# Kernel tuning notes

Hardware: AMD Instinct MI355X
Metric: run time of the kernel (lower is better)

## Reference

```python
import jax, jax.numpy as jnp
import numpy as np

H = 256  # hidden_size
B, LQ, LK = 4, 4096, 4096


def setup_inputs() -> dict:
    key = jax.random.key(0)
    ks = jax.random.split(key, 9)
    s = 1.0 / np.sqrt(H)
    return {
        "q": jax.random.normal(ks[0], (B, LQ, H), jnp.float32),
        "k": jax.random.normal(ks[1], (B, LK, H), jnp.float32),
        "v": jax.random.normal(ks[2], (B, LK, H), jnp.float32),
        "Wq": jax.random.uniform(ks[3], (H, H), jnp.float32, -s, s),
        "bq": jax.random.uniform(ks[4], (H,), jnp.float32, -s, s),
        "Wk": jax.random.uniform(ks[5], (H, H), jnp.float32, -s, s),
        "bk": jax.random.uniform(ks[6], (H,), jnp.float32, -s, s),
        "Wv": jax.random.uniform(ks[7], (H, H), jnp.float32, -s, s),
        "bv": jax.random.uniform(ks[8], (H,), jnp.float32, -s, s),
    }


def reference(q, k, v, Wq, bq, Wk, bk, Wv, bv):
    # Linear projections (torch Linear: x @ W.T + b)
    query = jnp.einsum('bsh,oh->bso', q, Wq) + bq
    keys = jnp.einsum('bsh,oh->bso', k, Wk) + bk
    values = jnp.einsum('bsh,oh->bso', v, Wv) + bv
    scores = jnp.einsum('bqh,bkh->bqk', query, keys) / jnp.sqrt(jnp.float32(H))
    weights = jax.nn.softmax(scores, axis=-1)
    context = jnp.einsum('bqk,bkh->bqh', weights, values)
    return context
```

## Files before the change

### kernel.cpp

```cpp
#include <hip/hip_runtime.h>
#include <hip/hip_bf16.h>
#include <stdint.h>

#define HD   256
#define SEQ  4096
#define NB   4
#define NTOK (NB * SEQ)
#define NEL  ((size_t)NTOK * HD)

typedef __hip_bfloat16 bf16;
typedef short    bf16x8  __attribute__((ext_vector_type(8)));
typedef float    f32x16  __attribute__((ext_vector_type(16)));
typedef float    f32x4_t __attribute__((ext_vector_type(4)));
typedef uint32_t u32x2_t __attribute__((ext_vector_type(2)));

__device__ __forceinline__ uint32_t pk2bf(float a, float b) {
  uint32_t ua = __builtin_bit_cast(uint32_t, a);
  uint32_t ub = __builtin_bit_cast(uint32_t, b);
  return ((ua + 0x8000u) >> 16) | ((ub + 0x8000u) & 0xFFFF0000u);
}
__device__ __forceinline__ uint16_t f2bf(float a) {
  uint32_t u = __builtin_bit_cast(uint32_t, a);
  return (uint16_t)((u + 0x8000u) >> 16);
}

__global__ __launch_bounds__(256, 2) void proj_kernel(
    const float* __restrict__ X, const float* __restrict__ W,
    const float* __restrict__ bias, bf16* __restrict__ out, float scale) {
  __shared__ bf16 xl[64][264];
  const int tid = (int)threadIdx.x;
  const int w = tid >> 6, l = tid & 63;
  const int m = l & 31, h = l >> 5;
  const int m0 = (int)blockIdx.x * 64;

#pragma unroll
  for (int j = 0; j < 16; ++j) {
    int e = j * 256 + tid;
    int row = e >> 6, c4 = e & 63;
    f32x4_t v = *(const f32x4_t*)(X + (size_t)(m0 + row) * HD + c4 * 4);
    u32x2_t pk; pk.x = pk2bf(v.x, v.y); pk.y = pk2bf(v.z, v.w);
    *(u32x2_t*)(&xl[row][c4 * 4]) = pk;
  }
  __syncthreads();

  f32x16 acc00 = {}, acc01 = {}, acc10 = {}, acc11 = {};

#pragma unroll
  for (int kh = 0; kh < 2; ++kh) {
    bf16x8 bfr[2][8];
#pragma unroll
    for (int nt2 = 0; nt2 < 2; ++nt2)
#pragma unroll
      for (int ks = 0; ks < 8; ++ks) {
        const float* wp = W + (size_t)(w * 64 + nt2 * 32 + m) * HD + (kh * 8 + ks) * 16 + h * 8;
        f32x4_t w0 = *(const f32x4_t*)wp;
        f32x4_t w1 = *(const f32x4_t*)(wp + 4);
        union { uint32_t u[4]; bf16x8 v; } cv;
        cv.u[0] = pk2bf(w0.x, w0.y); cv.u[1] = pk2bf(w0.z, w0.w);
        cv.u[2] = pk2bf(w1.x, w1.y); cv.u[3] = pk2bf(w1.z, w1.w);
        bfr[nt2][ks] = cv.v;
      }
#pragma unroll
    for (int ks = 0; ks < 8; ++ks) {
      int kbyte = (kh * 8 + ks) * 32 + h * 16;
      bf16x8 a0 = *(const bf16x8*)((const char*)&xl[m][0] + kbyte);
      bf16x8 a1 = *(const bf16x8*)((const char*)&xl[32 + m][0] + kbyte);
      acc00 = __builtin_amdgcn_mfma_f32_32x32x16_bf16(a0, bfr[0][ks], acc00, 0, 0, 0);
      acc01 = __builtin_amdgcn_mfma_f32_32x32x16_bf16(a0, bfr[1][ks], acc01, 0, 0, 0);
      acc10 = __builtin_amdgcn_mfma_f32_32x32x16_bf16(a1, bfr[0][ks], acc10, 0, 0, 0);
      acc11 = __builtin_amdgcn_mfma_f32_32x32x16_bf16(a1, bfr[1][ks], acc11, 0, 0, 0);
    }
  }
  __syncthreads();

  float bv0 = bias[w * 64 + m];
  float bv1 = bias[w * 64 + 32 + m];
#pragma unroll
  for (int r = 0; r < 16; ++r) {
    int row = (r & 3) + ((r >> 2) << 3) + 4 * h;
    xl[row][w * 64 + m]           = __builtin_bit_cast(bf16, f2bf((acc00[r] + bv0) * scale));
    xl[row][w * 64 + 32 + m]      = __builtin_bit_cast(bf16, f2bf((acc01[r] + bv1) * scale));
    xl[32 + row][w * 64 + m]      = __builtin_bit_cast(bf16, f2bf((acc10[r] + bv0) * scale));
    xl[32 + row][w * 64 + 32 + m] = __builtin_bit_cast(bf16, f2bf((acc11[r] + bv1) * scale));
  }
  __syncthreads();
#pragma unroll
  for (int j = 0; j < 8; ++j) {
    int unit = j * 256 + tid;
    int row = unit >> 5, uc = unit & 31;
    f32x4_t vv = *(const f32x4_t*)((const char*)&xl[row][0] + uc * 16);
    *(f32x4_t*)(out + (size_t)(m0 + row) * HD + uc * 8) = vv;
  }
}

__global__ __launch_bounds__(256, 2) void transpose_kernel(
    const bf16* __restrict__ Vp, bf16* __restrict__ Vt) {
  __shared__ bf16 tl[64][70];
  const int tid = (int)threadIdx.x;
  const int m0 = (int)blockIdx.x * 64, n0 = (int)blockIdx.y * 64;
  const int batch = m0 >> 12, s0 = m0 & (SEQ - 1);
#pragma unroll
  for (int j = 0; j < 4; ++j) {
    int unit = j * 256 + tid;
    int row = unit >> 4, qc = unit & 15;
    u32x2_t v = *(const u32x2_t*)(Vp + (size_t)(m0 + row) * HD + n0 + qc * 4);
    uint32_t* dst = (uint32_t*)&tl[row][qc * 4];
    dst[0] = v.x; dst[1] = v.y;
  }
  __syncthreads();
#pragma unroll
  for (int j = 0; j < 4; ++j) {
    int unit = j * 256 + tid;
    int orow = unit >> 4, oc = unit & 15;
    uint32_t w0 = (uint32_t)__builtin_bit_cast(uint16_t, tl[oc * 4 + 0][orow]) |
                  ((uint32_t)__builtin_bit_cast(uint16_t, tl[oc * 4 + 1][orow]) << 16);
    uint32_t w1 = (uint32_t)__builtin_bit_cast(uint16_t, tl[oc * 4 + 2][orow]) |
                  ((uint32_t)__builtin_bit_cast(uint16_t, tl[oc * 4 + 3][orow]) << 16);
    uint32_t* dst = (uint32_t*)(Vt + (size_t)batch * HD * SEQ + (size_t)(n0 + orow) * SEQ + s0 + oc * 4);
    dst[0] = w0; dst[1] = w1;
  }
}

__global__ __launch_bounds__(256, 2) void attn_kernel(
    const bf16* __restrict__ Qp, const bf16* __restrict__ Kp,
    const bf16* __restrict__ Vt, float* __restrict__ Op,
    float* __restrict__ Lp, int kvlen) {
  __shared__ __align__(128) char smem[65536];
  char* Kl = smem;
  char* Vl = smem + 32768;

  const int tid = (int)threadIdx.x;
  const int w = tid >> 6, l = tid & 63;
  const int m = l & 31, h = l >> 5;
  const int qt = (int)blockIdx.x, b = (int)blockIdx.y, sp = (int)blockIdx.z;
  const int kvbase = sp * kvlen;
  const int niter = kvlen >> 5;

  const int gq = b * SEQ + qt * 128 + w * 32 + m;
  bf16x8 qf[16];
#pragma unroll
  for (int ks = 0; ks < 16; ++ks)
    qf[ks] = *(const bf16x8*)(Qp + (size_t)gq * HD + ks * 16 + h * 8);

  f32x16 oacc[8] = {};
  float Lacc = 0.f;

  auto stage = [&](int buf, int kv0) {
#pragma unroll
    for (int i = 0; i < 4; ++i) {
      int kk = i * 8 + w * 2 + (l >> 5);
      int s = (l & 31) ^ (kk & 31);
      const bf16* src = Kp + (size_t)(b * SEQ + kv0 + kk) * HD + s * 8;
      __builtin_amdgcn_global_load_lds(
          (const __attribute__((address_space(1))) void*)src,
          (__attribute__((address_space(3))) void*)(Kl + buf * 16384 + i * 4096 + w * 1024),
          16, 0, 0);
    }
#pragma unroll
    for (int i = 0; i < 4; ++i) {
      int r = i * 32 + w * 8 + (l >> 3);
      int slog = (l & 7) ^ (r & 7);
      int d = r * 2 + (slog >> 2), j = slog & 3;
      const bf16* src = Vt + (size_t)b * HD * SEQ + (size_t)d * SEQ + kv0 + j * 8;
      __builtin_amdgcn_global_load_lds(
          (const __attribute__((address_space(1))) void*)src,
          (__attribute__((address_space(3))) void*)(Vl + buf * 16384 + i * 4096 + w * 1024),
          16, 0, 0);
    }
  };

  stage(0, kvbase);
  asm volatile("s_waitcnt vmcnt(0)" ::: "memory");
  __syncthreads();

  for (int t = 0; t < niter; ++t) {
    const int cur = t & 1;
    if (t + 1 < niter) stage(cur ^ 1, kvbase + (t + 1) * 32);

    f32x16 s0 = {};
    const char* kb = Kl + cur * 16384 + m * 512;
    __builtin_amdgcn_s_setprio(1);
#pragma unroll
    for (int ks = 0; ks < 16; ++ks) {
      bf16x8 k0 = *(const bf16x8*)(kb + (((2 * ks + h) ^ m) << 4));
      s0 = __builtin_amdgcn_mfma_f32_32x32x16_bf16(k0, qf[ks], s0, 0, 0, 0);
    }
    __builtin_amdgcn_s_setprio(0);

    float p[16];
#pragma unroll
    for (int r = 0; r < 16; ++r) p[r] = __builtin_exp2f(s0[r]);
    float ls = 0.f;
#pragma unroll
    for (int r = 0; r < 16; ++r) ls += p[r];
    Lacc += ls;

    bf16x8 pf[2];
#pragma unroll
    for (int ks = 0; ks < 2; ++ks) {
      int o = ks * 8;
      uint32_t P0, P1, P2, P3;
      asm("v_cvt_pk_bf16_f32 %0, %1, %2" : "=v"(P0) : "v"(p[o + 0]), "v"(p[o + 1]));
      asm("v_cvt_pk_bf16_f32 %0, %1, %2" : "=v"(P1) : "v"(p[o + 2]), "v"(p[o + 3]));
      asm("v_cvt_pk_bf16_f32 %0, %1, %2" : "=v"(P2) : "v"(p[o + 4]), "v"(p[o + 5]));
      asm("v_cvt_pk_bf16_f32 %0, %1, %2" : "=v"(P3) : "v"(p[o + 6]), "v"(p[o + 7]));
      asm volatile("v_permlane32_swap_b32 %0, %1" : "+v"(P0), "+v"(P2));
      asm volatile("v_permlane32_swap_b32 %0, %1" : "+v"(P1), "+v"(P3));
      union { uint32_t u[4]; bf16x8 v; } cv;
      cv.u[0] = P0; cv.u[1] = P1; cv.u[2] = P2; cv.u[3] = P3;
      pf[ks] = cv.v;
    }

    const char* vb = Vl + cur * 16384;
    __builtin_amdgcn_s_setprio(1);
#pragma unroll
    for (int dt = 0; dt < 8; ++dt) {
      int d = dt * 32 + m;
      int r = d >> 1;
#pragma unroll
      for (int ks = 0; ks < 2; ++ks) {
        int x = (((d & 1) << 2) | (2 * ks + h)) ^ (r & 7);
        bf16x8 vf = *(const bf16x8*)(vb + r * 128 + x * 16);
        oacc[dt] = __builtin_amdgcn_mfma_f32_32x32x16_bf16(vf, pf[ks], oacc[dt], 0, 0, 0);
      }
    }
    __builtin_amdgcn_s_setprio(0);

    asm volatile("s_waitcnt vmcnt(0)" ::: "memory");
    __syncthreads();
  }

  float Lrow = Lacc + __shfl_xor(Lacc, 32, 64);
  if (l < 32)
    Lp[(size_t)sp * NTOK + b * SEQ + qt * 128 + w * 32 + m] = Lrow;

#pragma unroll
  for (int half = 0; half < 2; ++half) {
    __syncthreads();
    if ((w >> 1) == half) {
      const int ql = (w & 1) * 32 + m;
#pragma unroll
      for (int dt = 0; dt < 8; ++dt)
#pragma unroll
        for (int rq = 0; rq < 4; ++rq) {
          int drow = dt * 32 + rq * 8 + 4 * h;
          f32x4_t vv;
          vv.x = oacc[dt][rq * 4 + 0]; vv.y = oacc[dt][rq * 4 + 1];
          vv.z = oacc[dt][rq * 4 + 2]; vv.w = oacc[dt][rq * 4 + 3];
          int slot = (drow >> 2) ^ (ql & 31);
          *(f32x4_t*)(smem + ql * 1024 + slot * 16) = vv;
        }
    }
    __syncthreads();
#pragma unroll
    for (int j = 0; j < 16; ++j) {
      int unit = j * 256 + tid;
      int qq = unit >> 6, sl = unit & 63;
      f32x4_t vv = *(const f32x4_t*)(smem + qq * 1024 + ((sl ^ (qq & 31)) << 4));
      int gqq = b * SEQ + qt * 128 + half * 64 + qq;
      *(f32x4_t*)(Op + (size_t)sp * NEL + (size_t)gqq * HD + sl * 4) = vv;
    }
  }
}

__global__ __launch_bounds__(256, 2) void combine_kernel(
    const float* __restrict__ Op, const float* __restrict__ Lp,
    float* __restrict__ out, int nsplit) {
  size_t qd = (size_t)blockIdx.x * 256 + threadIdx.x;
  int row = (int)(qd >> 6);
  f32x4_t v = ((const f32x4_t*)Op)[qd];
  float Ls = Lp[row];
  for (int s = 1; s < nsplit; ++s) {
    f32x4_t v2 = ((const f32x4_t*)Op)[qd + (size_t)s * (NEL >> 2)];
    v.x += v2.x; v.y += v2.y; v.z += v2.z; v.w += v2.w;
    Ls += Lp[(size_t)s * NTOK + row];
  }
  float inv = 1.f / Ls;
  v.x *= inv; v.y *= inv; v.z *= inv; v.w *= inv;
  ((f32x4_t*)out)[qd] = v;
}

extern "C" void kernel_launch(void* const* d_in, const int* in_sizes, int n_in,
                              void* d_out, int out_size, void* d_ws, size_t ws_size,
                              hipStream_t stream) {
  (void)in_sizes; (void)n_in; (void)out_size;
  const float* q  = (const float*)d_in[0];
  const float* k  = (const float*)d_in[1];
  const float* v  = (const float*)d_in[2];
  const float* Wq = (const float*)d_in[3];
  const float* bq = (const float*)d_in[4];
  const float* Wk = (const float*)d_in[5];
  const float* bk = (const float*)d_in[6];
  const float* Wv = (const float*)d_in[7];
  const float* bv = (const float*)d_in[8];

  char* ws = (char*)d_ws;
  bf16* Qp = (bf16*)ws;
  bf16* Kp = Qp + NEL;
  bf16* Vp = Kp + NEL;
  bf16* Vt = Vp + NEL;
  float* Op = (float*)(ws + 4 * NEL * sizeof(bf16));

  int nsplit = 1;
  for (int cand = 4; cand > 1; cand >>= 1) {
    size_t need = 4 * NEL * sizeof(bf16) + (size_t)cand * NEL * sizeof(float) +
                  (size_t)cand * NTOK * sizeof(float);
    if (ws_size >= need) { nsplit = cand; break; }
  }
  float* Lp = Op + (size_t)nsplit * NEL;

  const float CEXP = 0.09016844f;

  proj_kernel<<<NTOK / 64, 256, 0, stream>>>(q, Wq, bq, Qp, CEXP);
  proj_kernel<<<NTOK / 64, 256, 0, stream>>>(k, Wk, bk, Kp, 1.0f);
  proj_kernel<<<NTOK / 64, 256, 0, stream>>>(v, Wv, bv, Vp, 1.0f);
  transpose_kernel<<<dim3(NTOK / 64, HD / 64), 256, 0, stream>>>(Vp, Vt);
  attn_kernel<<<dim3(SEQ / 128, NB, nsplit), 256, 0, stream>>>(Qp, Kp, Vt, Op, Lp, SEQ / nsplit);
  combine_kernel<<<(int)((NEL / 4) / 256), 256, 0, stream>>>(Op, Lp, (float*)d_out, nsplit);
}
```

Baseline: 142.4 us.

## Merge QKV projections into one launch and relax attention pipeline waits

The three projection launches become one 3D-grid launch that picks its input, weights and bias by blockIdx.y. In the attention loop, the full vmcnt(0) wait plus syncthreads at the end of each iteration is replaced by barriers around the prefetch, with vmcnt(8). This lets the next tile's loads stay in flight while the current tile is consumed. The V tile's LDS swizzle changes from 128-byte rows with an 8-way XOR to 256-byte rows with a 16-way XOR, to reduce bank conflicts. The risks are the correctness of the partial waitcnt and the new swizzle mapping.

Measured after the change: 136.1 us. 4.4% less time.

```diff
diff --git a/kernel.cpp b/kernel.cpp
--- a/kernel.cpp
+++ b/kernel.cpp
@@ -25,8 +25,17 @@
 }
 
 __global__ __launch_bounds__(256, 2) void proj_kernel(
-    const float* __restrict__ X, const float* __restrict__ W,
-    const float* __restrict__ bias, bf16* __restrict__ out, float scale) {
+    const float* __restrict__ Xq, const float* __restrict__ Xk, const float* __restrict__ Xv,
+    const float* __restrict__ Wq, const float* __restrict__ Wk, const float* __restrict__ Wv,
+    const float* __restrict__ bq, const float* __restrict__ bk, const float* __restrict__ bv,
+    bf16* __restrict__ out0, float cexp) {
+  const int which = (int)blockIdx.y;
+  const float* X    = which == 0 ? Xq : which == 1 ? Xk : Xv;
+  const float* W    = which == 0 ? Wq : which == 1 ? Wk : Wv;
+  const float* bias = which == 0 ? bq : which == 1 ? bk : bv;
+  bf16* out = out0 + (size_t)which * NEL;
+  const float scale = which == 0 ? cexp : 1.0f;
+
   __shared__ bf16 xl[64][264];
   const int tid = (int)threadIdx.x;
   const int w = tid >> 6, l = tid & 63;
@@ -158,9 +167,9 @@
     }
 #pragma unroll
     for (int i = 0; i < 4; ++i) {
-      int r = i * 32 + w * 8 + (l >> 3);
-      int slog = (l & 7) ^ (r & 7);
-      int d = r * 2 + (slog >> 2), j = slog & 3;
+      int r = i * 16 + w * 4 + (l >> 4);
+      int x = (l & 15) ^ (r & 15);
+      int d = (r << 2) + (x >> 2), j = x & 3;
       const bf16* src = Vt + (size_t)b * HD * SEQ + (size_t)d * SEQ + kv0 + j * 8;
       __builtin_amdgcn_global_load_lds(
           (const __attribute__((address_space(1))) void*)src,
@@ -170,12 +179,18 @@
   };
 
   stage(0, kvbase);
-  asm volatile("s_waitcnt vmcnt(0)" ::: "memory");
-  __syncthreads();
 
   for (int t = 0; t < niter; ++t) {
     const int cur = t & 1;
-    if (t + 1 < niter) stage(cur ^ 1, kvbase + (t + 1) * 32);
+
+    asm volatile("s_barrier" ::: "memory");
+    if (t + 1 < niter) {
+      stage(cur ^ 1, kvbase + (t + 1) * 32);
+      asm volatile("s_waitcnt vmcnt(8)" ::: "memory");
+    } else {
+      asm volatile("s_waitcnt vmcnt(0)" ::: "memory");
+    }
+    asm volatile("s_barrier" ::: "memory");
 
     f32x16 s0 = {};
     const char* kb = Kl + cur * 16384 + m * 512;
@@ -216,18 +231,15 @@
 #pragma unroll
     for (int dt = 0; dt < 8; ++dt) {
       int d = dt * 32 + m;
-      int r = d >> 1;
+      int r = d >> 2;
 #pragma unroll
       for (int ks = 0; ks < 2; ++ks) {
-        int x = (((d & 1) << 2) | (2 * ks + h)) ^ (r & 7);
-        bf16x8 vf = *(const bf16x8*)(vb + r * 128 + x * 16);
+        int x = (((d & 3) << 2) | (2 * ks + h)) ^ (r & 15);
+        bf16x8 vf = *(const bf16x8*)(vb + r * 256 + x * 16);
         oacc[dt] = __builtin_amdgcn_mfma_f32_32x32x16_bf16(vf, pf[ks], oacc[dt], 0, 0, 0);
       }
     }
     __builtin_amdgcn_s_setprio(0);
-
-    asm volatile("s_waitcnt vmcnt(0)" ::: "memory");
-    __syncthreads();
   }
 
   float Lrow = Lacc + __shfl_xor(Lacc, 32, 64);
@@ -296,9 +308,9 @@
 
   char* ws = (char*)d_ws;
   bf16* Qp = (bf16*)ws;
+  bf16* Vp = Qp + 2 * NEL;
+  bf16* Vt = Vp + NEL;
   bf16* Kp = Qp + NEL;
-  bf16* Vp = Kp + NEL;
-  bf16* Vt = Vp + NEL;
   float* Op = (float*)(ws + 4 * NEL * sizeof(bf16));
 
   int nsplit = 1;
@@ -311,9 +323,7 @@
 
   const float CEXP = 0.09016844f;
 
-  proj_kernel<<<NTOK / 64, 256, 0, stream>>>(q, Wq, bq, Qp, CEXP);
-  proj_kernel<<<NTOK / 64, 256, 0, stream>>>(k, Wk, bk, Kp, 1.0f);
-  proj_kernel<<<NTOK / 64, 256, 0, stream>>>(v, Wv, bv, Vp, 1.0f);
+  proj_kernel<<<dim3(NTOK / 64, 3), 256, 0, stream>>>(q, k, v, Wq, Wk, Wv, bq, bk, bv, Qp, CEXP);
   transpose_kernel<<<dim3(NTOK / 64, HD / 64), 256, 0, stream>>>(Vp, Vt);
   attn_kernel<<<dim3(SEQ / 128, NB, nsplit), 256, 0, stream>>>(Qp, Kp, Vt, Op, Lp, SEQ / nsplit);
   combine_kernel<<<(int)((NEL / 4) / 256), 256, 0, stream>>>(Op, Lp, (float*)d_out, nsplit);
```
